# Optimization experiments

Measured on AMD Instinct MI355X. Metric: run time of the kernel, lower is better.

The kernel has to match this reference:

```python
import jax, jax.numpy as jnp
import numpy as np
import math

N_CELLS = 8192
IN_DIM = 64
HID = 128
OUT_DIM = 64
MAX_AGE = 50.0
TOP_K = 8


def faction_sync_debate(h, step, n_factions=8, sync_strength=0.15, debate_strength=0.15):
    n, d = h.shape
    n_f = min(n_factions, n // 2)
    if n_f < 2:
        return h
    fs = n // n_f
    used = n_f * fs
    body = h[:used].reshape(n_f, fs, d)
    fmean = body.mean(axis=1, keepdims=True)                 # per-faction mean
    body = (1.0 - sync_strength) * body + sync_strength * fmean
    if step > 5:
        global_op = body.mean(axis=1).mean(axis=0)           # [d]
        dc = max(1, fs // 4)
        body = body.at[:, :dc].set((1.0 - debate_strength) * body[:, :dc] + debate_strength * global_op)
    out = body.reshape(used, d)
    if used < n:
        out = jnp.concatenate([out, h[used:]], axis=0)
    return out


def setup_inputs() -> dict:
    key = jax.random.key(0)
    ks = jax.random.split(key, 10)

    def lin(k, fin, fout):
        kw, kb = jax.random.split(k)
        s = 1.0 / math.sqrt(fin)
        w = jax.random.uniform(kw, (fout, fin), minval=-s, maxval=s, dtype=jnp.float32)
        b = jax.random.uniform(kb, (fout,), minval=-s, maxval=s, dtype=jnp.float32)
        return w, b

    in_w, in_b = lin(ks[0], IN_DIM, HID)
    out_w, out_b = lin(ks[1], HID, IN_DIM)
    ea_w1, ea_b1 = lin(ks[2], HID, 128)
    ea_w2, ea_b2 = lin(ks[3], 128, OUT_DIM)
    eg_w1, eg_b1 = lin(ks[4], HID, 128)
    eg_w2, eg_b2 = lin(ks[5], 128, OUT_DIM)
    prototypes = jax.random.normal(ks[6], (N_CELLS, HID), dtype=jnp.float32) * 0.3
    # sparse random topology state (evolved-state stand-in for the zero-init buffers)
    edges = (jax.random.uniform(ks[7], (N_CELLS, N_CELLS)) < 0.001).astype(jnp.float32)
    edges = jnp.maximum(edges, edges.T)
    edge_ages = jax.random.randint(ks[8], (N_CELLS, N_CELLS), 0, 60).astype(jnp.float32) * edges
    x = jax.random.normal(ks[9], (1, IN_DIM), dtype=jnp.float32)
    return dict(x=x, step=10, prototypes=prototypes, edges=edges, edge_ages=edge_ages,
                in_w=in_w, in_b=in_b, out_w=out_w, out_b=out_b,
                ea_w1=ea_w1, ea_b1=ea_b1, ea_w2=ea_w2, ea_b2=ea_b2,
                eg_w1=eg_w1, eg_b1=eg_b1, eg_w2=eg_w2, eg_b2=eg_b2)


def reference(x, step, prototypes, edges, edge_ages, in_w, in_b, out_w, out_b,
              ea_w1, ea_b1, ea_w2, ea_b2, eg_w1, eg_b1, eg_w2, eg_b2):
    signal = (x @ in_w.T + in_b)[0]                          # [HID]
    # ---- torch.no_grad() region: GNG competitive update ----
    sgp = jax.lax.stop_gradient(prototypes)
    sgs = jax.lax.stop_gradient(signal)
    dists = jnp.sum((sgp - sgs[None, :]) ** 2, axis=-1)      # [N]
    sorted_idx = jnp.argsort(dists)
    bmu1, bmu2 = sorted_idx[0], sorted_idx[1]
    eps_w = max(0.05, 0.3 * math.exp(-step / 200.0))
    eps_n = eps_w * 0.01
    proto = sgp.at[bmu1].add(eps_w * (sgs - sgp[bmu1]))
    proto = proto.at[bmu2].add(eps_n * (sgs - proto[bmu2]))
    e = edges.at[bmu1, bmu2].set(1.0).at[bmu2, bmu1].set(1.0)
    ages = edge_ages.at[bmu1, bmu2].set(0.0).at[bmu2, bmu1].set(0.0)
    ages = ages.at[bmu1, :].add(1.0).at[:, bmu1].add(1.0)
    old = ages > MAX_AGE
    e = jnp.where(old, 0.0, e)
    ages = jnp.where(old, 0.0, ages)
    # vectorized neighbor EMA (replaces per-neighbor python loop; rows independent)
    nmask = (e[bmu1] > 0).astype(proto.dtype)                # [N]
    proto = proto + eps_n * nmask[:, None] * (sgs[None, :] - proto)
    proto = faction_sync_debate(proto, step)
    # value = updated prototypes, grad = identity to the prototypes parameter
    # (torch mutates .data in-place, then reads the Parameter directly)
    proto_used = prototypes + jax.lax.stop_gradient(proto - prototypes)
    # ---- differentiable head ----
    winner_h = proto_used[bmu1][None, :]                     # [1, HID]
    a_out = jax.nn.relu(winner_h @ ea_w1.T + ea_b1) @ ea_w2.T + ea_b2
    g_out = jax.nn.relu(winner_h @ eg_w1.T + eg_b1) @ eg_w2.T + eg_b2
    tension = jnp.mean((a_out - g_out) ** 2)
    top_idx = sorted_idx[:TOP_K]
    weights = jax.nn.softmax(-dists[top_idx])                # [K]
    combined = jnp.sum(weights[:, None] * proto_used[top_idx], axis=0, keepdims=True)
    output = combined @ out_w.T + out_b                      # [1, IN_DIM]
    return output, tension
```

## Files before the change

kernel.cpp:

```cpp
#include <hip/hip_runtime.h>
#include <math.h>

#define N_CELLS 8192
#define HIDDIM 128
#define IN_DIM 64
#define TOPK 8


__global__ void k_init(float* __restrict__ z) {
    int t = blockIdx.x * blockDim.x + threadIdx.x;
    if (t < 2056) z[t] = 0.0f;
}

__global__ __launch_bounds__(128) void k_signal(const float* __restrict__ x,
                                                const float* __restrict__ in_w,
                                                const float* __restrict__ in_b,
                                                float* __restrict__ signal) {
    int j = threadIdx.x;
    float acc = in_b[j];
    const float* w = in_w + j * IN_DIM;
    #pragma unroll
    for (int k = 0; k < IN_DIM; ++k) acc += x[k] * w[k];
    signal[j] = acc;
}

__global__ __launch_bounds__(256) void k_dist(const float* __restrict__ proto,
                                              const float* __restrict__ signal,
                                              float* __restrict__ dists,
                                              float* __restrict__ fsum0) {
    __shared__ float sm[4 * 128];
    int tid = threadIdx.x;
    int wave = tid >> 6, lane = tid & 63;
    float2 s2 = ((const float2*)signal)[lane];
    float fx = 0.0f, fy = 0.0f;
    int base = blockIdx.x * 64;
    for (int c = wave; c < 64; c += 4) {
        int cell = base + c;
        float2 p = ((const float2*)(proto + (size_t)cell * HIDDIM))[lane];
        float dx = p.x - s2.x, dy = p.y - s2.y;
        float d = dx * dx + dy * dy;
        #pragma unroll
        for (int off = 32; off > 0; off >>= 1) d += __shfl_down(d, off, 64);
        if (lane == 0) dists[cell] = d;
        fx += p.x; fy += p.y;
    }
    sm[wave * 128 + 2 * lane]     = fx;
    sm[wave * 128 + 2 * lane + 1] = fy;
    __syncthreads();
    if (tid < 128) {
        float s = sm[tid] + sm[128 + tid] + sm[256 + tid] + sm[384 + tid];
        int f = blockIdx.x >> 4;
        atomicAdd(&fsum0[f * HIDDIM + tid], s);
    }
}

__global__ __launch_bounds__(256) void k_top8(const float* __restrict__ dists,
                                              float* __restrict__ topdist,
                                              int* __restrict__ topidx) {
    __shared__ float sd[N_CELLS];
    __shared__ float sv[256];
    __shared__ int   si[256];
    int tid = threadIdx.x;
    for (int j = 0; j < 32; ++j) sd[j * 256 + tid] = dists[j * 256 + tid];
    __syncthreads();
    for (int k = 0; k < TOPK; ++k) {
        float lv = INFINITY; int li = N_CELLS;
        #pragma unroll
        for (int j = 0; j < 32; ++j) {
            int   ii = j * 256 + tid;
            float vv = sd[ii];
            if (vv < lv || (vv == lv && ii < li)) { lv = vv; li = ii; }
        }
        sv[tid] = lv; si[tid] = li;
        __syncthreads();
        for (int s = 128; s > 0; s >>= 1) {
            if (tid < s) {
                float ov = sv[tid + s]; int oi = si[tid + s];
                if (ov < sv[tid] || (ov == sv[tid] && oi < si[tid])) { sv[tid] = ov; si[tid] = oi; }
            }
            __syncthreads();
        }
        if (tid == 0) {
            topdist[k] = sv[0];
            topidx[k]  = si[0];
            sd[si[0]]  = INFINITY;
        }
        __syncthreads();
    }
}

__global__ __launch_bounds__(256) void k_coef(const float* __restrict__ proto,
                                              const float* __restrict__ edges,
                                              const float* __restrict__ ages,
                                              const int* __restrict__ step_p,
                                              const int* __restrict__ topidx,
                                              float* __restrict__ acoef,
                                              float* __restrict__ csum,
                                              float* __restrict__ Bf) {
    int i = blockIdx.x * blockDim.x + threadIdx.x;
    if (i >= N_CELLS) return;
    int bmu1 = topidx[0], bmu2 = topidx[1];
    float step = (float)step_p[0];
    float eps_w = fmaxf(0.05f, 0.3f * expf(-step / 200.0f));
    float eps_n = eps_w * 0.01f;

    size_t ro = (size_t)bmu1 * N_CELLS + (size_t)i;
    float age, ec;
    if (i == bmu2)      { age = 1.0f;             ec = 1.0f; }
    else if (i == bmu1) { age = ages[ro] + 2.0f;  ec = edges[ro]; }
    else                { age = ages[ro] + 1.0f;  ec = edges[ro]; }
    bool nb = ((age > 50.0f) ? 0.0f : ec) > 0.0f;

    float a = 1.0f;
    if (i == bmu1) a *= (1.0f - eps_w);
    if (i == bmu2) a *= (1.0f - eps_n);
    if (nb)        a *= (1.0f - eps_n);
    acoef[i] = a;

    if (a != 1.0f) {
        int f = i >> 10;
        const float* p = proto + (size_t)i * HIDDIM;
        for (int d = 0; d < HIDDIM; ++d)
            atomicAdd(&csum[f * HIDDIM + d], (a - 1.0f) * p[d]);
        atomicAdd(&Bf[f], 1.0f - a);
    }
}

__global__ __launch_bounds__(128) void k_final(const float* __restrict__ proto,
                                               const float* __restrict__ signal,
                                               const float* __restrict__ acoef,
                                               const float* __restrict__ fsum0,
                                               const float* __restrict__ csum,
                                               const float* __restrict__ Bf,
                                               const float* __restrict__ topdist,
                                               const int* __restrict__ topidx,
                                               const int* __restrict__ step_p,
                                               const float* __restrict__ ea_w1,
                                               const float* __restrict__ ea_b1,
                                               const float* __restrict__ ea_w2,
                                               const float* __restrict__ ea_b2,
                                               const float* __restrict__ eg_w1,
                                               const float* __restrict__ eg_b1,
                                               const float* __restrict__ eg_w2,
                                               const float* __restrict__ eg_b2,
                                               const float* __restrict__ out_w,
                                               const float* __restrict__ out_b,
                                               float* __restrict__ d_out) {
    __shared__ float wh[128], cmb[128], hA[128], hG[128];
    int d = threadIdx.x;
    int step = step_p[0];
    float s = signal[d];

    float fm[8]; float g = 0.0f;
    #pragma unroll
    for (int f = 0; f < 8; ++f) {
        float v = (fsum0[f * 128 + d] + csum[f * 128 + d] + Bf[f] * s) * (1.0f / 1024.0f);
        fm[f] = v; g += v;
    }
    g *= (1.0f / 8.0f);

    float w[TOPK]; float tot = 0.0f; float m = topdist[0];
    #pragma unroll
    for (int k = 0; k < TOPK; ++k) { w[k] = expf(-(topdist[k] - m)); tot += w[k]; }
    float inv = 1.0f / tot;

    float comb = 0.0f, win = 0.0f;
    #pragma unroll
    for (int k = 0; k < TOPK; ++k) {
        int idx = topidx[k];
        float a  = acoef[idx];
        float p1 = a * proto[(size_t)idx * 128 + d] + (1.0f - a) * s;
        float pf = 0.85f * p1 + 0.15f * fm[idx >> 10];
        if (step > 5 && (idx & 1023) < 256) pf = 0.85f * pf + 0.15f * g;
        comb += (w[k] * inv) * pf;
        if (k == 0) win = pf;
    }
    wh[d] = win; cmb[d] = comb;
    __syncthreads();

    float ha = ea_b1[d], hg = eg_b1[d];
    for (int j = 0; j < 128; ++j) {
        ha += wh[j] * ea_w1[d * 128 + j];
        hg += wh[j] * eg_w1[d * 128 + j];
    }
    hA[d] = fmaxf(ha, 0.0f);
    hG[d] = fmaxf(hg, 0.0f);
    __syncthreads();

    if (d < 64) {
        float ao = ea_b2[d], go = eg_b2[d], ov = out_b[d];
        for (int j = 0; j < 128; ++j) {
            ao += hA[j] * ea_w2[d * 128 + j];
            go += hG[j] * eg_w2[d * 128 + j];
            ov += cmb[j] * out_w[d * 128 + j];
        }
        d_out[d] = ov;
        float diff = ao - go;
        float sq = diff * diff;
        #pragma unroll
        for (int off = 32; off > 0; off >>= 1) sq += __shfl_down(sq, off, 64);
        if (d == 0) d_out[64] = sq * (1.0f / 64.0f);
    }
}

extern "C" void kernel_launch(void* const* d_in, const int* in_sizes, int n_in,
                              void* d_out, int out_size, void* d_ws, size_t ws_size,
                              hipStream_t stream) {
    (void)in_sizes; (void)n_in; (void)out_size; (void)ws_size;
    const float* x      = (const float*)d_in[0];
    const int*   step_p = (const int*)  d_in[1];
    const float* proto  = (const float*)d_in[2];
    const float* edges  = (const float*)d_in[3];
    const float* ages   = (const float*)d_in[4];
    const float* in_w   = (const float*)d_in[5];
    const float* in_b   = (const float*)d_in[6];
    const float* out_w  = (const float*)d_in[7];
    const float* out_b  = (const float*)d_in[8];
    const float* ea_w1  = (const float*)d_in[9];
    const float* ea_b1  = (const float*)d_in[10];
    const float* ea_w2  = (const float*)d_in[11];
    const float* ea_b2  = (const float*)d_in[12];
    const float* eg_w1  = (const float*)d_in[13];
    const float* eg_b1  = (const float*)d_in[14];
    const float* eg_w2  = (const float*)d_in[15];
    const float* eg_b2  = (const float*)d_in[16];

    float* ws     = (float*)d_ws;
    float* signal = ws;
    float* dists  = ws + 128;
    float* acoef  = ws + 8320;
    float* fsum0  = ws + 16512;
    float* csum   = ws + 17536;
    float* Bf     = ws + 18560;
    float* topd   = ws + 18568;
    int*   topi   = (int*)(ws + 18576);
    float* out    = (float*)d_out;

    k_init  <<<dim3(9),   dim3(256), 0, stream>>>(fsum0);
    k_signal<<<dim3(1),   dim3(128), 0, stream>>>(x, in_w, in_b, signal);
    k_dist  <<<dim3(128), dim3(256), 0, stream>>>(proto, signal, dists, fsum0);
    k_top8  <<<dim3(1),   dim3(256), 0, stream>>>(dists, topd, topi);
    k_coef  <<<dim3(32),  dim3(256), 0, stream>>>(proto, edges, ages, step_p, topi, acoef, csum, Bf);
    k_final <<<dim3(1),   dim3(128), 0, stream>>>(proto, signal, acoef, fsum0, csum, Bf, topd, topi, step_p,
                                                  ea_w1, ea_b1, ea_w2, ea_b2,
                                                  eg_w1, eg_b1, eg_w2, eg_b2,
                                                  out_w, out_b, out);
}
```

Baseline: 492.3 us.

## Fuse six kernels into distance kernel plus single-block tail kernel

Collapses the pipeline from six launches to two. The input projection is recomputed inside each distance block, so the separate signal kernel goes away. Faction sums are written as per-block partials instead of global atomics, which removes the zero-init kernel. Top-8 selection, coefficient and neighbour computation, and the MLP head now run in one single-block kernel, with the coefficients and faction corrections held in shared-memory atomics. This trades launch overhead and global round-trips for serial work in a single block, notably the coefficient pass over all 8192 cells.

```diff
diff --git a/kernel.cpp b/kernel.cpp
--- a/kernel.cpp
+++ b/kernel.cpp
@@ -7,37 +7,32 @@
 #define TOPK 8
 
 
-__global__ void k_init(float* __restrict__ z) {
-    int t = blockIdx.x * blockDim.x + threadIdx.x;
-    if (t < 2056) z[t] = 0.0f;
-}
-
-__global__ __launch_bounds__(128) void k_signal(const float* __restrict__ x,
-                                                const float* __restrict__ in_w,
-                                                const float* __restrict__ in_b,
-                                                float* __restrict__ signal) {
-    int j = threadIdx.x;
-    float acc = in_b[j];
-    const float* w = in_w + j * IN_DIM;
-    #pragma unroll
-    for (int k = 0; k < IN_DIM; ++k) acc += x[k] * w[k];
-    signal[j] = acc;
-}
-
-__global__ __launch_bounds__(256) void k_dist(const float* __restrict__ proto,
-                                              const float* __restrict__ signal,
+__global__ __launch_bounds__(256) void k_dist(const float* __restrict__ x,
+                                              const float* __restrict__ in_w,
+                                              const float* __restrict__ in_b,
+                                              const float* __restrict__ proto,
                                               float* __restrict__ dists,
-                                              float* __restrict__ fsum0) {
+                                              float* __restrict__ fpart) {
+    __shared__ float sig[HIDDIM];
     __shared__ float sm[4 * 128];
     int tid = threadIdx.x;
+    if (tid < HIDDIM) {
+        float acc = in_b[tid];
+        const float* w = in_w + tid * IN_DIM;
+        #pragma unroll
+        for (int k = 0; k < IN_DIM; ++k) acc += x[k] * w[k];
+        sig[tid] = acc;
+    }
+    __syncthreads();
+
     int wave = tid >> 6, lane = tid & 63;
-    float2 s2 = ((const float2*)signal)[lane];
+    float sx = sig[2 * lane], sy = sig[2 * lane + 1];
     float fx = 0.0f, fy = 0.0f;
     int base = blockIdx.x * 64;
     for (int c = wave; c < 64; c += 4) {
         int cell = base + c;
         float2 p = ((const float2*)(proto + (size_t)cell * HIDDIM))[lane];
-        float dx = p.x - s2.x, dy = p.y - s2.y;
+        float dx = p.x - sx, dy = p.y - sy;
         float d = dx * dx + dy * dy;
         #pragma unroll
         for (int off = 32; off > 0; off >>= 1) d += __shfl_down(d, off, 64);
@@ -49,18 +44,44 @@
     __syncthreads();
     if (tid < 128) {
         float s = sm[tid] + sm[128 + tid] + sm[256 + tid] + sm[384 + tid];
-        int f = blockIdx.x >> 4;
-        atomicAdd(&fsum0[f * HIDDIM + tid], s);
+        fpart[blockIdx.x * 128 + tid] = s;
     }
 }
 
-__global__ __launch_bounds__(256) void k_top8(const float* __restrict__ dists,
-                                              float* __restrict__ topdist,
-                                              int* __restrict__ topidx) {
+__global__ __launch_bounds__(256) void k_rest(const float* __restrict__ proto,
+                                              const float* __restrict__ x,
+                                              const float* __restrict__ in_w,
+                                              const float* __restrict__ in_b,
+                                              const float* __restrict__ dists,
+                                              const float* __restrict__ fpart,
+                                              const float* __restrict__ edges,
+                                              const float* __restrict__ ages,
+                                              const int* __restrict__ step_p,
+                                              const float* __restrict__ ea_w1,
+                                              const float* __restrict__ ea_b1,
+                                              const float* __restrict__ ea_w2,
+                                              const float* __restrict__ ea_b2,
+                                              const float* __restrict__ eg_w1,
+                                              const float* __restrict__ eg_b1,
+                                              const float* __restrict__ eg_w2,
+                                              const float* __restrict__ eg_b2,
+                                              const float* __restrict__ out_w,
+                                              const float* __restrict__ out_b,
+                                              float* __restrict__ d_out) {
     __shared__ float sd[N_CELLS];
     __shared__ float sv[256];
     __shared__ int   si[256];
+    __shared__ float topd_s[TOPK];
+    __shared__ int   topi_s[TOPK];
+    __shared__ float csum_s[8 * HIDDIM];
+    __shared__ float Bf_s[8];
+    __shared__ float wh[128], cmb[128], hA[128], hG[128];
+
     int tid = threadIdx.x;
+
+    for (int j = tid; j < 8 * HIDDIM; j += 256) csum_s[j] = 0.0f;
+    if (tid < 8) Bf_s[tid] = 0.0f;
+
     for (int j = 0; j < 32; ++j) sd[j * 256 + tid] = dists[j * 256 + tid];
     __syncthreads();
     for (int k = 0; k < TOPK; ++k) {
@@ -81,113 +102,92 @@
             __syncthreads();
         }
         if (tid == 0) {
-            topdist[k] = sv[0];
-            topidx[k]  = si[0];
-            sd[si[0]]  = INFINITY;
+            topd_s[k] = sv[0];
+            topi_s[k] = si[0];
+            sd[si[0]] = INFINITY;
         }
         __syncthreads();
     }
-}
-
-__global__ __launch_bounds__(256) void k_coef(const float* __restrict__ proto,
-                                              const float* __restrict__ edges,
-                                              const float* __restrict__ ages,
-                                              const int* __restrict__ step_p,
-                                              const int* __restrict__ topidx,
-                                              float* __restrict__ acoef,
-                                              float* __restrict__ csum,
-                                              float* __restrict__ Bf) {
-    int i = blockIdx.x * blockDim.x + threadIdx.x;
-    if (i >= N_CELLS) return;
-    int bmu1 = topidx[0], bmu2 = topidx[1];
-    float step = (float)step_p[0];
-    float eps_w = fmaxf(0.05f, 0.3f * expf(-step / 200.0f));
+
+    int bmu1 = topi_s[0], bmu2 = topi_s[1];
+    float stepf = (float)step_p[0];
+    float eps_w = fmaxf(0.05f, 0.3f * expf(-stepf / 200.0f));
     float eps_n = eps_w * 0.01f;
-
-    size_t ro = (size_t)bmu1 * N_CELLS + (size_t)i;
-    float age, ec;
-    if (i == bmu2)      { age = 1.0f;             ec = 1.0f; }
-    else if (i == bmu1) { age = ages[ro] + 2.0f;  ec = edges[ro]; }
-    else                { age = ages[ro] + 1.0f;  ec = edges[ro]; }
-    bool nb = ((age > 50.0f) ? 0.0f : ec) > 0.0f;
-
-    float a = 1.0f;
-    if (i == bmu1) a *= (1.0f - eps_w);
-    if (i == bmu2) a *= (1.0f - eps_n);
-    if (nb)        a *= (1.0f - eps_n);
-    acoef[i] = a;
-
-    if (a != 1.0f) {
-        int f = i >> 10;
-        const float* p = proto + (size_t)i * HIDDIM;
-        for (int d = 0; d < HIDDIM; ++d)
-            atomicAdd(&csum[f * HIDDIM + d], (a - 1.0f) * p[d]);
-        atomicAdd(&Bf[f], 1.0f - a);
-    }
-}
-
-__global__ __launch_bounds__(128) void k_final(const float* __restrict__ proto,
-                                               const float* __restrict__ signal,
-                                               const float* __restrict__ acoef,
-                                               const float* __restrict__ fsum0,
-                                               const float* __restrict__ csum,
-                                               const float* __restrict__ Bf,
-                                               const float* __restrict__ topdist,
-                                               const int* __restrict__ topidx,
-                                               const int* __restrict__ step_p,
-                                               const float* __restrict__ ea_w1,
-                                               const float* __restrict__ ea_b1,
-                                               const float* __restrict__ ea_w2,
-                                               const float* __restrict__ ea_b2,
-                                               const float* __restrict__ eg_w1,
-                                               const float* __restrict__ eg_b1,
-                                               const float* __restrict__ eg_w2,
-                                               const float* __restrict__ eg_b2,
-                                               const float* __restrict__ out_w,
-                                               const float* __restrict__ out_b,
-                                               float* __restrict__ d_out) {
-    __shared__ float wh[128], cmb[128], hA[128], hG[128];
-    int d = threadIdx.x;
+    for (int j = 0; j < 32; ++j) {
+        int i = j * 256 + tid;
+        size_t ro = (size_t)bmu1 * N_CELLS + (size_t)i;
+        float age, ec;
+        if (i == bmu2)      { age = 1.0f;             ec = 1.0f; }
+        else if (i == bmu1) { age = ages[ro] + 2.0f;  ec = edges[ro]; }
+        else                { age = ages[ro] + 1.0f;  ec = edges[ro]; }
+        bool nb = ((age > 50.0f) ? 0.0f : ec) > 0.0f;
+        float a = 1.0f;
+        if (i == bmu1) a *= (1.0f - eps_w);
+        if (i == bmu2) a *= (1.0f - eps_n);
+        if (nb)        a *= (1.0f - eps_n);
+        sd[i] = a;
+        if (a != 1.0f) {
+            int f = i >> 10;
+            const float* p = proto + (size_t)i * HIDDIM;
+            for (int d2 = 0; d2 < HIDDIM; ++d2)
+                atomicAdd(&csum_s[f * HIDDIM + d2], (a - 1.0f) * p[d2]);
+            atomicAdd(&Bf_s[f], 1.0f - a);
+        }
+    }
+    __syncthreads();
+
     int step = step_p[0];
-    float s = signal[d];
-
-    float fm[8]; float g = 0.0f;
-    #pragma unroll
-    for (int f = 0; f < 8; ++f) {
-        float v = (fsum0[f * 128 + d] + csum[f * 128 + d] + Bf[f] * s) * (1.0f / 1024.0f);
-        fm[f] = v; g += v;
-    }
-    g *= (1.0f / 8.0f);
-
-    float w[TOPK]; float tot = 0.0f; float m = topdist[0];
-    #pragma unroll
-    for (int k = 0; k < TOPK; ++k) { w[k] = expf(-(topdist[k] - m)); tot += w[k]; }
-    float inv = 1.0f / tot;
-
-    float comb = 0.0f, win = 0.0f;
-    #pragma unroll
-    for (int k = 0; k < TOPK; ++k) {
-        int idx = topidx[k];
-        float a  = acoef[idx];
-        float p1 = a * proto[(size_t)idx * 128 + d] + (1.0f - a) * s;
-        float pf = 0.85f * p1 + 0.15f * fm[idx >> 10];
-        if (step > 5 && (idx & 1023) < 256) pf = 0.85f * pf + 0.15f * g;
-        comb += (w[k] * inv) * pf;
-        if (k == 0) win = pf;
-    }
-    wh[d] = win; cmb[d] = comb;
-    __syncthreads();
-
-    float ha = ea_b1[d], hg = eg_b1[d];
-    for (int j = 0; j < 128; ++j) {
-        ha += wh[j] * ea_w1[d * 128 + j];
-        hg += wh[j] * eg_w1[d * 128 + j];
-    }
-    hA[d] = fmaxf(ha, 0.0f);
-    hG[d] = fmaxf(hg, 0.0f);
-    __syncthreads();
-
-    if (d < 64) {
+    if (tid < 128) {
+        int d = tid;
+        float s = in_b[d];
+        const float* w = in_w + d * IN_DIM;
+        #pragma unroll
+        for (int k = 0; k < IN_DIM; ++k) s += x[k] * w[k];
+
+        float fm[8]; float g = 0.0f;
+        #pragma unroll
+        for (int f = 0; f < 8; ++f) {
+            float acc = csum_s[f * HIDDIM + d] + Bf_s[f] * s;
+            for (int b = 0; b < 16; ++b) acc += fpart[(f * 16 + b) * 128 + d];
+            float v = acc * (1.0f / 1024.0f);
+            fm[f] = v; g += v;
+        }
+        g *= (1.0f / 8.0f);
+
+        float wgt[TOPK]; float tot = 0.0f; float m = topd_s[0];
+        #pragma unroll
+        for (int k = 0; k < TOPK; ++k) { wgt[k] = expf(-(topd_s[k] - m)); tot += wgt[k]; }
+        float inv = 1.0f / tot;
+
+        float comb = 0.0f, win = 0.0f;
+        #pragma unroll
+        for (int k = 0; k < TOPK; ++k) {
+            int idx = topi_s[k];
+            float a  = sd[idx];
+            float p1 = a * proto[(size_t)idx * HIDDIM + d] + (1.0f - a) * s;
+            float pf = 0.85f * p1 + 0.15f * fm[idx >> 10];
+            if (step > 5 && (idx & 1023) < 256) pf = 0.85f * pf + 0.15f * g;
+            comb += (wgt[k] * inv) * pf;
+            if (k == 0) win = pf;
+        }
+        wh[d] = win; cmb[d] = comb;
+    }
+    __syncthreads();
+
+    {
+        int d = tid & 127;
+        const float* w1 = (tid < 128) ? ea_w1 : eg_w1;
+        const float* b1 = (tid < 128) ? ea_b1 : eg_b1;
+        float h = b1[d];
+        const float* wr = w1 + d * 128;
+        for (int j = 0; j < 128; ++j) h += wh[j] * wr[j];
+        if (tid < 128) hA[d] = fmaxf(h, 0.0f);
+        else           hG[d] = fmaxf(h, 0.0f);
+    }
+    __syncthreads();
+
+    if (tid < 64) {
+        int d = tid;
         float ao = ea_b2[d], go = eg_b2[d], ov = out_b[d];
         for (int j = 0; j < 128; ++j) {
             ao += hA[j] * ea_w2[d * 128 + j];
@@ -225,24 +225,15 @@
     const float* eg_w2  = (const float*)d_in[15];
     const float* eg_b2  = (const float*)d_in[16];
 
-    float* ws     = (float*)d_ws;
-    float* signal = ws;
-    float* dists  = ws + 128;
-    float* acoef  = ws + 8320;
-    float* fsum0  = ws + 16512;
-    float* csum   = ws + 17536;
-    float* Bf     = ws + 18560;
-    float* topd   = ws + 18568;
-    int*   topi   = (int*)(ws + 18576);
-    float* out    = (float*)d_out;
-
-    k_init  <<<dim3(9),   dim3(256), 0, stream>>>(fsum0);
-    k_signal<<<dim3(1),   dim3(128), 0, stream>>>(x, in_w, in_b, signal);
-    k_dist  <<<dim3(128), dim3(256), 0, stream>>>(proto, signal, dists, fsum0);
-    k_top8  <<<dim3(1),   dim3(256), 0, stream>>>(dists, topd, topi);
-    k_coef  <<<dim3(32),  dim3(256), 0, stream>>>(proto, edges, ages, step_p, topi, acoef, csum, Bf);
-    k_final <<<dim3(1),   dim3(128), 0, stream>>>(proto, signal, acoef, fsum0, csum, Bf, topd, topi, step_p,
-                                                  ea_w1, ea_b1, ea_w2, ea_b2,
-                                                  eg_w1, eg_b1, eg_w2, eg_b2,
-                                                  out_w, out_b, out);
+    float* ws    = (float*)d_ws;
+    float* dists = ws;
+    float* fpart = ws + N_CELLS;
+    float* out   = (float*)d_out;
+
+    k_dist<<<dim3(128), dim3(256), 0, stream>>>(x, in_w, in_b, proto, dists, fpart);
+    k_rest<<<dim3(1),   dim3(256), 0, stream>>>(proto, x, in_w, in_b, dists, fpart,
+                                                edges, ages, step_p,
+                                                ea_w1, ea_b1, ea_w2, ea_b2,
+                                                eg_w1, eg_b1, eg_w2, eg_b2,
+                                                out_w, out_b, out);
 }
```

After: 514.6 us. 1.05x slower.
